# Performance work log

Hardware: AMD Instinct MI355X
Metric: run time of the kernel (lower is better)

Reference implementation:

```python
import jax, jax.numpy as jnp
import numpy as np

N, D_IN, D_OUT = 4096, 1024, 1024


def setup_inputs() -> dict:
    key = jax.random.key(0)
    kx, kq, kk, kv = jax.random.split(key, 4)
    s = 1.0 / np.sqrt(D_IN)
    return {
        "x": jax.random.normal(kx, (N, D_IN), dtype=jnp.float32),
        "Wq": jax.random.normal(kq, (D_OUT, D_IN), dtype=jnp.float32) * s,
        "Wk": jax.random.normal(kk, (D_OUT, D_IN), dtype=jnp.float32) * s,
        "Wv": jax.random.normal(kv, (D_OUT, D_IN), dtype=jnp.float32) * s,
    }


def reference(x, Wq, Wk, Wv):
    # nn.Linear(d_in, d_out, bias=False): y = x @ W.T with W: [d_out, d_in]
    q = x @ Wq.T            # [N, d_out]
    k = x @ Wk.T            # [N, d_out]
    v = x @ Wv.T            # [N, d_out]
    scores = q @ k.T        # [N, N]
    scale = 1.0 / jnp.sqrt(jnp.asarray(k.shape[-1], dtype=x.dtype))
    attn = jax.nn.softmax(scores * scale, axis=-1)
    return attn @ v         # [N, d_out]
```

## Files before the change

### kernel.cpp

```cpp
#include <hip/hip_runtime.h>


typedef __attribute__((ext_vector_type(8))) __bf16 bf16x8;
typedef __attribute__((ext_vector_type(4))) float floatx4;

#define GLB_AS __attribute__((address_space(1)))
#define LDS_AS __attribute__((address_space(3)))

static __device__ __forceinline__ unsigned short f2bf_u16(float f) {
  union { float f; unsigned u; } x; x.f = f;
  unsigned r = x.u;
  r += 0x7fffu + ((r >> 16) & 1u);
  return (unsigned short)(r >> 16);
}
static __device__ __forceinline__ float bf2f(unsigned short u) {
  union { unsigned u; float f; } x; x.u = ((unsigned)u) << 16; return x.f;
}

__global__ __launch_bounds__(256) void cast_all(const float* __restrict__ x,
                                                const float* __restrict__ Wq,
                                                const float* __restrict__ Wk,
                                                const float* __restrict__ Wv,
                                                unsigned short* __restrict__ xb,
                                                unsigned short* __restrict__ wb) {
  const int i = blockIdx.x * 256 + threadIdx.x;
  const int NX4 = 4096 * 1024 / 4;
  const int NW4 = 1024 * 1024 / 4;
  const float* src; unsigned short* dst; int k;
  if (i < NX4)                { src = x;  dst = xb;                   k = i; }
  else if (i < NX4 + NW4)     { src = Wq; dst = wb;                   k = i - NX4; }
  else if (i < NX4 + 2 * NW4) { src = Wk; dst = wb + 1024 * 1024;     k = i - NX4 - NW4; }
  else                        { src = Wv; dst = wb + 2 * 1024 * 1024; k = i - NX4 - 2 * NW4; }
  float4 v = reinterpret_cast<const float4*>(src)[k];
  ushort4 o = make_ushort4(f2bf_u16(v.x), f2bf_u16(v.y), f2bf_u16(v.z), f2bf_u16(v.w));
  reinterpret_cast<ushort4*>(dst)[k] = o;
}

struct GemmOuts { void* c[4]; int ldc[4]; };

template <int EPI>
__global__ __launch_bounds__(256, 4) void gemm128(const unsigned short* __restrict__ A,
                                                  const unsigned short* __restrict__ B,
                                                  GemmOuts outs, int lda, int ldb,
                                                  int klen, float scale) {
  __shared__ unsigned short sh[16384];
  const int t = threadIdx.x;
  const int w = t >> 6, lane = t & 63;
  const int wm = w >> 1, wn = w & 1;
  const int gx = gridDim.x;
  const int nwg = gx * gridDim.y;
  int bid = blockIdx.y * gx + blockIdx.x;
  bid = (bid & 7) * (nwg >> 3) + (bid >> 3);
  const int row0 = (bid / gx) * 128;
  const int col0 = (bid % gx) * 128;
  const int z = blockIdx.z;
  const int kstart = z * klen;
  const int NT = klen >> 5;

  const int srow = t >> 2;
  const int scbe = (((t & 3) ^ ((t >> 3) & 3)) << 3);
  const unsigned short* gA0 = A + (size_t)(row0 + srow) * lda + kstart + scbe;
  const unsigned short* gA1 = gA0 + (size_t)64 * lda;
  const unsigned short* gB0 = B + (size_t)(col0 + srow) * ldb + kstart + scbe;
  const unsigned short* gB1 = gB0 + (size_t)64 * ldb;

#define STAGE(tl_) do { \
    const int bb_ = ((tl_) & 1) * 8192; \
    __builtin_amdgcn_global_load_lds((const GLB_AS void*)(gA0 + (tl_) * 32), \
        (LDS_AS void*)&sh[bb_ + t * 8], 16, 0, 0); \
    __builtin_amdgcn_global_load_lds((const GLB_AS void*)(gA1 + (tl_) * 32), \
        (LDS_AS void*)&sh[bb_ + 2048 + t * 8], 16, 0, 0); \
    __builtin_amdgcn_global_load_lds((const GLB_AS void*)(gB0 + (tl_) * 32), \
        (LDS_AS void*)&sh[bb_ + 4096 + t * 8], 16, 0, 0); \
    __builtin_amdgcn_global_load_lds((const GLB_AS void*)(gB1 + (tl_) * 32), \
        (LDS_AS void*)&sh[bb_ + 6144 + t * 8], 16, 0, 0); \
  } while (0)

  const int fr = lane & 15;
  const int sg = (((lane >> 4) ^ ((lane >> 1) & 3)) << 3);
  int aofs[4], bofs[4];
#pragma unroll
  for (int mf = 0; mf < 4; ++mf) aofs[mf] = ((wm * 64 + mf * 16 + fr) << 5) + sg;
#pragma unroll
  for (int nf = 0; nf < 4; ++nf) bofs[nf] = 4096 + ((wn * 64 + nf * 16 + fr) << 5) + sg;

  floatx4 acc[4][4] = {};

  STAGE(0);

  for (int tile = 0; tile < NT; ++tile) {
    if (tile + 1 < NT) {
      STAGE(tile + 1);
      asm volatile("s_waitcnt vmcnt(4)" ::: "memory");
    } else {
      asm volatile("s_waitcnt vmcnt(0)" ::: "memory");
    }
    __builtin_amdgcn_s_barrier();

    const int bo = (tile & 1) * 8192;
    bf16x8 af[4], bf[4];
#pragma unroll
    for (int mf = 0; mf < 4; ++mf) af[mf] = *(const bf16x8*)&sh[bo + aofs[mf]];
#pragma unroll
    for (int nf = 0; nf < 4; ++nf) bf[nf] = *(const bf16x8*)&sh[bo + bofs[nf]];
#pragma unroll
    for (int mf = 0; mf < 4; ++mf)
#pragma unroll
      for (int nf = 0; nf < 4; ++nf)
        acc[mf][nf] = __builtin_amdgcn_mfma_f32_16x16x32_bf16(af[mf], bf[nf], acc[mf][nf], 0, 0, 0);

    __builtin_amdgcn_s_barrier();
  }
#undef STAGE

  const int er = (lane >> 4) * 4;
  const int ec = lane & 15;

  if (EPI == 0) {
    unsigned short* Cb = (unsigned short*)outs.c[z];
    const int ldc = outs.ldc[z];
#pragma unroll
    for (int mf = 0; mf < 4; ++mf)
#pragma unroll
      for (int nf = 0; nf < 4; ++nf)
#pragma unroll
        for (int r = 0; r < 4; ++r)
          Cb[(size_t)(row0 + wm * 64 + mf * 16 + er + r) * ldc +
             (col0 + wn * 64 + nf * 16 + ec)] = f2bf_u16(acc[mf][nf][r] * scale);
  } else if (EPI == 2) {
    unsigned short* Pb = (unsigned short*)outs.c[0];
    float* rsp = (float*)outs.c[1];
    const int ldc = outs.ldc[0];
    const int rj = ((col0 >> 7) * 2 + wn) * 4096;
#pragma unroll
    for (int mf = 0; mf < 4; ++mf) {
#pragma unroll
      for (int r = 0; r < 4; ++r) {
        const int m = row0 + wm * 64 + mf * 16 + er + r;
        float rsum = 0.f;
#pragma unroll
        for (int nf = 0; nf < 4; ++nf) {
          const float e = __expf(acc[mf][nf][r] * scale);
          Pb[(size_t)m * ldc + (col0 + wn * 64 + nf * 16 + ec)] = f2bf_u16(e);
          rsum += e;
        }
        rsum += __shfl_xor(rsum, 1);
        rsum += __shfl_xor(rsum, 2);
        rsum += __shfl_xor(rsum, 4);
        rsum += __shfl_xor(rsum, 8);
        if (ec == 0) rsp[rj + m] = rsum;
      }
    }
  } else {
    if (col0 < 2048) {
      unsigned short* qkb = (unsigned short*)outs.c[0];
#pragma unroll
      for (int mf = 0; mf < 4; ++mf)
#pragma unroll
        for (int nf = 0; nf < 4; ++nf)
#pragma unroll
          for (int r = 0; r < 4; ++r)
            qkb[(size_t)(row0 + wm * 64 + mf * 16 + er + r) * 2048 +
                (col0 + wn * 64 + nf * 16 + ec)] = f2bf_u16(acc[mf][nf][r] * scale);
    } else {
      unsigned short* vT = (unsigned short*)outs.c[1];
#pragma unroll
      for (int mf = 0; mf < 4; ++mf)
#pragma unroll
        for (int nf = 0; nf < 4; ++nf) {
          const int n = (col0 - 2048) + wn * 64 + nf * 16 + ec;
          const int mb = row0 + wm * 64 + mf * 16 + er;
          ushort4 o = make_ushort4(f2bf_u16(acc[mf][nf][0] * scale),
                                   f2bf_u16(acc[mf][nf][1] * scale),
                                   f2bf_u16(acc[mf][nf][2] * scale),
                                   f2bf_u16(acc[mf][nf][3] * scale));
          *reinterpret_cast<ushort4*>(&vT[(size_t)n * 4096 + mb]) = o;
        }
    }
  }
}

__global__ __launch_bounds__(256) void reduce_pv(float* __restrict__ out,
                                                 const unsigned short* __restrict__ p0,
                                                 const unsigned short* __restrict__ p1,
                                                 const unsigned short* __restrict__ p2,
                                                 const unsigned short* __restrict__ p3,
                                                 const float* __restrict__ rsp) {
  const int row = blockIdx.x;
  const int lane = threadIdx.x & 63;
  float s = rsp[lane * 4096 + row];
#pragma unroll
  for (int off = 32; off >= 1; off >>= 1) s += __shfl_xor(s, off);
  const float inv = 1.0f / s;
  const int idx = row * 256 + threadIdx.x;
  ushort4 a = ((const ushort4*)p0)[idx];
  ushort4 b = ((const ushort4*)p1)[idx];
  ushort4 c = ((const ushort4*)p2)[idx];
  ushort4 d = ((const ushort4*)p3)[idx];
  float4 o;
  o.x = (bf2f(a.x) + bf2f(b.x) + bf2f(c.x) + bf2f(d.x)) * inv;
  o.y = (bf2f(a.y) + bf2f(b.y) + bf2f(c.y) + bf2f(d.y)) * inv;
  o.z = (bf2f(a.z) + bf2f(b.z) + bf2f(c.z) + bf2f(d.z)) * inv;
  o.w = (bf2f(a.w) + bf2f(b.w) + bf2f(c.w) + bf2f(d.w)) * inv;
  ((float4*)out)[idx] = o;
}

extern "C" void kernel_launch(void* const* d_in, const int* in_sizes, int n_in,
                              void* d_out, int out_size, void* d_ws, size_t ws_size,
                              hipStream_t stream) {
  const float* x  = (const float*)d_in[0];
  const float* Wq = (const float*)d_in[1];
  const float* Wk = (const float*)d_in[2];
  const float* Wv = (const float*)d_in[3];
  float* out = (float*)d_out;

  const int N = 4096, D = 1024;

  char* ws = (char*)d_ws;
  unsigned short* P   = (unsigned short*)ws;
  unsigned short* qkb = (unsigned short*)(ws + (32u << 20));
  unsigned short* vT  = (unsigned short*)(ws + (48u << 20));
  unsigned short* xb  = (unsigned short*)(ws + (56u << 20));
  unsigned short* wb  = (unsigned short*)(ws + (64u << 20));
  float*          rsp = (float*)(ws + (70u << 20));
  unsigned short* p0  = xb;
  unsigned short* p1  = (unsigned short*)(ws + (72u << 20));
  unsigned short* p2  = (unsigned short*)(ws + (80u << 20));
  unsigned short* p3  = (unsigned short*)(ws + (88u << 20));

  cast_all<<<7168, 256, 0, stream>>>(x, Wq, Wk, Wv, xb, wb);

  GemmOuts oq; oq.c[0] = qkb; oq.c[1] = vT; oq.c[2] = oq.c[3] = qkb;
  oq.ldc[0] = 2048; oq.ldc[1] = 4096; oq.ldc[2] = oq.ldc[3] = 2048;
  gemm128<3><<<dim3(3 * D / 128, N / 128, 1), 256, 0, stream>>>(xb, wb, oq, D, D, D, 1.0f);

  GemmOuts os; os.c[0] = P; os.c[1] = rsp; os.c[2] = os.c[3] = P;
  os.ldc[0] = N; os.ldc[1] = 0; os.ldc[2] = os.ldc[3] = N;
  gemm128<2><<<dim3(N / 128, N / 128, 1), 256, 0, stream>>>(qkb, qkb + D, os, 2 * D, 2 * D, D, 0.03125f);

  GemmOuts op;
  op.c[0] = p0; op.ldc[0] = D;
  op.c[1] = p1; op.ldc[1] = D;
  op.c[2] = p2; op.ldc[2] = D;
  op.c[3] = p3; op.ldc[3] = D;
  gemm128<0><<<dim3(D / 128, N / 128, 4), 256, 0, stream>>>(P, vT, op, N, N, N / 4, 1.0f);

  reduce_pv<<<N, 256, 0, stream>>>(out, p0, p1, p2, p3, rsp);
}
```

Baseline: 153.1 us.

## Enlarge GEMM tiles to 256x128 and halve split-K for PV

All three GEMMs now use a 256x128 output tile per workgroup: each wave computes 128x64 with 8x4 MFMA fragments, LDS staging grows to 24576 elements, and occupancy is declared as 2 workgroups per CU. The larger tile raises operand reuse from LDS and cuts global traffic per FLOP. The PV GEMM's split-K drops from 4 to 2, so the reduction kernel reads only two partial buffers. The trade-off is more register pressure, lower occupancy, fewer workgroups per grid (less parallelism) and longer epilogues.

Result: faster. 142.8 us (-6.7%).

```diff
diff --git a/kernel.cpp b/kernel.cpp
--- a/kernel.cpp
+++ b/kernel.cpp
@@ -39,11 +39,11 @@
 struct GemmOuts { void* c[4]; int ldc[4]; };
 
 template <int EPI>
-__global__ __launch_bounds__(256, 4) void gemm128(const unsigned short* __restrict__ A,
+__global__ __launch_bounds__(256, 2) void gemm_bt(const unsigned short* __restrict__ A,
                                                   const unsigned short* __restrict__ B,
                                                   GemmOuts outs, int lda, int ldb,
                                                   int klen, float scale) {
-  __shared__ unsigned short sh[16384];
+  __shared__ unsigned short sh[24576];
   const int t = threadIdx.x;
   const int w = t >> 6, lane = t & 63;
   const int wm = w >> 1, wn = w & 1;
@@ -51,7 +51,7 @@
   const int nwg = gx * gridDim.y;
   int bid = blockIdx.y * gx + blockIdx.x;
   bid = (bid & 7) * (nwg >> 3) + (bid >> 3);
-  const int row0 = (bid / gx) * 128;
+  const int row0 = (bid / gx) * 256;
   const int col0 = (bid % gx) * 128;
   const int z = blockIdx.z;
   const int kstart = z * klen;
@@ -61,50 +61,56 @@
   const int scbe = (((t & 3) ^ ((t >> 3) & 3)) << 3);
   const unsigned short* gA0 = A + (size_t)(row0 + srow) * lda + kstart + scbe;
   const unsigned short* gA1 = gA0 + (size_t)64 * lda;
+  const unsigned short* gA2 = gA0 + (size_t)128 * lda;
+  const unsigned short* gA3 = gA0 + (size_t)192 * lda;
   const unsigned short* gB0 = B + (size_t)(col0 + srow) * ldb + kstart + scbe;
   const unsigned short* gB1 = gB0 + (size_t)64 * ldb;
 
 #define STAGE(tl_) do { \
-    const int bb_ = ((tl_) & 1) * 8192; \
+    const int bb_ = ((tl_) & 1) * 12288; \
     __builtin_amdgcn_global_load_lds((const GLB_AS void*)(gA0 + (tl_) * 32), \
         (LDS_AS void*)&sh[bb_ + t * 8], 16, 0, 0); \
     __builtin_amdgcn_global_load_lds((const GLB_AS void*)(gA1 + (tl_) * 32), \
         (LDS_AS void*)&sh[bb_ + 2048 + t * 8], 16, 0, 0); \
+    __builtin_amdgcn_global_load_lds((const GLB_AS void*)(gA2 + (tl_) * 32), \
+        (LDS_AS void*)&sh[bb_ + 4096 + t * 8], 16, 0, 0); \
+    __builtin_amdgcn_global_load_lds((const GLB_AS void*)(gA3 + (tl_) * 32), \
+        (LDS_AS void*)&sh[bb_ + 6144 + t * 8], 16, 0, 0); \
     __builtin_amdgcn_global_load_lds((const GLB_AS void*)(gB0 + (tl_) * 32), \
-        (LDS_AS void*)&sh[bb_ + 4096 + t * 8], 16, 0, 0); \
+        (LDS_AS void*)&sh[bb_ + 8192 + t * 8], 16, 0, 0); \
     __builtin_amdgcn_global_load_lds((const GLB_AS void*)(gB1 + (tl_) * 32), \
-        (LDS_AS void*)&sh[bb_ + 6144 + t * 8], 16, 0, 0); \
+        (LDS_AS void*)&sh[bb_ + 10240 + t * 8], 16, 0, 0); \
   } while (0)
 
   const int fr = lane & 15;
   const int sg = (((lane >> 4) ^ ((lane >> 1) & 3)) << 3);
-  int aofs[4], bofs[4];
-#pragma unroll
-  for (int mf = 0; mf < 4; ++mf) aofs[mf] = ((wm * 64 + mf * 16 + fr) << 5) + sg;
-#pragma unroll
-  for (int nf = 0; nf < 4; ++nf) bofs[nf] = 4096 + ((wn * 64 + nf * 16 + fr) << 5) + sg;
-
-  floatx4 acc[4][4] = {};
+  int aofs[8], bofs[4];
+#pragma unroll
+  for (int mf = 0; mf < 8; ++mf) aofs[mf] = ((wm * 128 + mf * 16 + fr) << 5) + sg;
+#pragma unroll
+  for (int nf = 0; nf < 4; ++nf) bofs[nf] = 8192 + ((wn * 64 + nf * 16 + fr) << 5) + sg;
+
+  floatx4 acc[8][4] = {};
 
   STAGE(0);
 
   for (int tile = 0; tile < NT; ++tile) {
     if (tile + 1 < NT) {
       STAGE(tile + 1);
-      asm volatile("s_waitcnt vmcnt(4)" ::: "memory");
+      asm volatile("s_waitcnt vmcnt(6)" ::: "memory");
     } else {
       asm volatile("s_waitcnt vmcnt(0)" ::: "memory");
     }
     __builtin_amdgcn_s_barrier();
 
-    const int bo = (tile & 1) * 8192;
-    bf16x8 af[4], bf[4];
-#pragma unroll
-    for (int mf = 0; mf < 4; ++mf) af[mf] = *(const bf16x8*)&sh[bo + aofs[mf]];
+    const int bo = (tile & 1) * 12288;
+    bf16x8 af[8], bf[4];
+#pragma unroll
+    for (int mf = 0; mf < 8; ++mf) af[mf] = *(const bf16x8*)&sh[bo + aofs[mf]];
 #pragma unroll
     for (int nf = 0; nf < 4; ++nf) bf[nf] = *(const bf16x8*)&sh[bo + bofs[nf]];
 #pragma unroll
-    for (int mf = 0; mf < 4; ++mf)
+    for (int mf = 0; mf < 8; ++mf)
 #pragma unroll
       for (int nf = 0; nf < 4; ++nf)
         acc[mf][nf] = __builtin_amdgcn_mfma_f32_16x16x32_bf16(af[mf], bf[nf], acc[mf][nf], 0, 0, 0);
@@ -120,12 +126,12 @@
     unsigned short* Cb = (unsigned short*)outs.c[z];
     const int ldc = outs.ldc[z];
 #pragma unroll
-    for (int mf = 0; mf < 4; ++mf)
+    for (int mf = 0; mf < 8; ++mf)
 #pragma unroll
       for (int nf = 0; nf < 4; ++nf)
 #pragma unroll
         for (int r = 0; r < 4; ++r)
-          Cb[(size_t)(row0 + wm * 64 + mf * 16 + er + r) * ldc +
+          Cb[(size_t)(row0 + wm * 128 + mf * 16 + er + r) * ldc +
              (col0 + wn * 64 + nf * 16 + ec)] = f2bf_u16(acc[mf][nf][r] * scale);
   } else if (EPI == 2) {
     unsigned short* Pb = (unsigned short*)outs.c[0];
@@ -133,10 +139,10 @@
     const int ldc = outs.ldc[0];
     const int rj = ((col0 >> 7) * 2 + wn) * 4096;
 #pragma unroll
-    for (int mf = 0; mf < 4; ++mf) {
+    for (int mf = 0; mf < 8; ++mf) {
 #pragma unroll
       for (int r = 0; r < 4; ++r) {
-        const int m = row0 + wm * 64 + mf * 16 + er + r;
+        const int m = row0 + wm * 128 + mf * 16 + er + r;
         float rsum = 0.f;
 #pragma unroll
         for (int nf = 0; nf < 4; ++nf) {
@@ -155,21 +161,21 @@
     if (col0 < 2048) {
       unsigned short* qkb = (unsigned short*)outs.c[0];
 #pragma unroll
-      for (int mf = 0; mf < 4; ++mf)
+      for (int mf = 0; mf < 8; ++mf)
 #pragma unroll
         for (int nf = 0; nf < 4; ++nf)
 #pragma unroll
           for (int r = 0; r < 4; ++r)
-            qkb[(size_t)(row0 + wm * 64 + mf * 16 + er + r) * 2048 +
+            qkb[(size_t)(row0 + wm * 128 + mf * 16 + er + r) * 2048 +
                 (col0 + wn * 64 + nf * 16 + ec)] = f2bf_u16(acc[mf][nf][r] * scale);
     } else {
       unsigned short* vT = (unsigned short*)outs.c[1];
 #pragma unroll
-      for (int mf = 0; mf < 4; ++mf)
+      for (int mf = 0; mf < 8; ++mf)
 #pragma unroll
         for (int nf = 0; nf < 4; ++nf) {
           const int n = (col0 - 2048) + wn * 64 + nf * 16 + ec;
-          const int mb = row0 + wm * 64 + mf * 16 + er;
+          const int mb = row0 + wm * 128 + mf * 16 + er;
           ushort4 o = make_ushort4(f2bf_u16(acc[mf][nf][0] * scale),
                                    f2bf_u16(acc[mf][nf][1] * scale),
                                    f2bf_u16(acc[mf][nf][2] * scale),
@@ -183,8 +189,6 @@
 __global__ __launch_bounds__(256) void reduce_pv(float* __restrict__ out,
                                                  const unsigned short* __restrict__ p0,
                                                  const unsigned short* __restrict__ p1,
-                                                 const unsigned short* __restrict__ p2,
-                                                 const unsigned short* __restrict__ p3,
                                                  const float* __restrict__ rsp) {
   const int row = blockIdx.x;
   const int lane = threadIdx.x & 63;
@@ -195,13 +199,11 @@
   const int idx = row * 256 + threadIdx.x;
   ushort4 a = ((const ushort4*)p0)[idx];
   ushort4 b = ((const ushort4*)p1)[idx];
-  ushort4 c = ((const ushort4*)p2)[idx];
-  ushort4 d = ((const ushort4*)p3)[idx];
   float4 o;
-  o.x = (bf2f(a.x) + bf2f(b.x) + bf2f(c.x) + bf2f(d.x)) * inv;
-  o.y = (bf2f(a.y) + bf2f(b.y) + bf2f(c.y) + bf2f(d.y)) * inv;
-  o.z = (bf2f(a.z) + bf2f(b.z) + bf2f(c.z) + bf2f(d.z)) * inv;
-  o.w = (bf2f(a.w) + bf2f(b.w) + bf2f(c.w) + bf2f(d.w)) * inv;
+  o.x = (bf2f(a.x) + bf2f(b.x)) * inv;
+  o.y = (bf2f(a.y) + bf2f(b.y)) * inv;
+  o.z = (bf2f(a.z) + bf2f(b.z)) * inv;
+  o.w = (bf2f(a.w) + bf2f(b.w)) * inv;
   ((float4*)out)[idx] = o;
 }
 
@@ -225,25 +227,23 @@
   float*          rsp = (float*)(ws + (70u << 20));
   unsigned short* p0  = xb;
   unsigned short* p1  = (unsigned short*)(ws + (72u << 20));
-  unsigned short* p2  = (unsigned short*)(ws + (80u << 20));
-  unsigned short* p3  = (unsigned short*)(ws + (88u << 20));
 
   cast_all<<<7168, 256, 0, stream>>>(x, Wq, Wk, Wv, xb, wb);
 
   GemmOuts oq; oq.c[0] = qkb; oq.c[1] = vT; oq.c[2] = oq.c[3] = qkb;
   oq.ldc[0] = 2048; oq.ldc[1] = 4096; oq.ldc[2] = oq.ldc[3] = 2048;
-  gemm128<3><<<dim3(3 * D / 128, N / 128, 1), 256, 0, stream>>>(xb, wb, oq, D, D, D, 1.0f);
+  gemm_bt<3><<<dim3(3 * D / 128, N / 256, 1), 256, 0, stream>>>(xb, wb, oq, D, D, D, 1.0f);
 
   GemmOuts os; os.c[0] = P; os.c[1] = rsp; os.c[2] = os.c[3] = P;
   os.ldc[0] = N; os.ldc[1] = 0; os.ldc[2] = os.ldc[3] = N;
-  gemm128<2><<<dim3(N / 128, N / 128, 1), 256, 0, stream>>>(qkb, qkb + D, os, 2 * D, 2 * D, D, 0.03125f);
+  gemm_bt<2><<<dim3(N / 128, N / 256, 1), 256, 0, stream>>>(qkb, qkb + D, os, 2 * D, 2 * D, D, 0.03125f);
 
   GemmOuts op;
   op.c[0] = p0; op.ldc[0] = D;
   op.c[1] = p1; op.ldc[1] = D;
-  op.c[2] = p2; op.ldc[2] = D;
-  op.c[3] = p3; op.ldc[3] = D;
-  gemm128<0><<<dim3(D / 128, N / 128, 4), 256, 0, stream>>>(P, vT, op, N, N, N / 4, 1.0f);
-
-  reduce_pv<<<N, 256, 0, stream>>>(out, p0, p1, p2, p3, rsp);
-}
+  op.c[2] = p0; op.ldc[2] = D;
+  op.c[3] = p1; op.ldc[3] = D;
+  gemm_bt<0><<<dim3(D / 128, N / 256, 2), 256, 0, stream>>>(P, vT, op, N, N, N / 2, 1.0f);
+
+  reduce_pv<<<N, 256, 0, stream>>>(out, p0, p1, rsp);
+}
```
